# Kernel optimization log

Measured on AMD Instinct MI355X. Metric: run time of the kernel, lower is better.

## Reference

```python
import jax, jax.numpy as jnp
import numpy as np

A_, BS, T, V, E, H, NA = 8, 32, 256, 128, 512, 512, 64

def setup_inputs() -> dict:
    key = jax.random.key(0)
    ks = jax.random.split(key, 6)
    def w(k, shape, fan):
        return (jax.random.normal(k, shape, jnp.float32) / np.sqrt(fan)).astype(jnp.float32)
    return {
        "x": jax.random.normal(ks[0], (A_, BS, T, V), jnp.float32),
        "hidden_states": jnp.zeros((A_, BS, 1, H), jnp.float32),
        "enc_w": w(ks[1], (E, V), V),
        "enc_b": jnp.zeros((E,), jnp.float32),
        "w_ih": w(ks[2], (3 * H, E), E),
        "w_hh": w(ks[3], (3 * H, H), H),
        "b_ih": jnp.zeros((3 * H,), jnp.float32),
        "b_hh": jnp.zeros((3 * H,), jnp.float32),
        "dec_w": w(ks[4], (NA, H), H),
        "dec_b": jnp.zeros((NA,), jnp.float32),
    }

def _gru_scan(enc_t, h0, w_ih, w_hh, b_ih, b_hh):
    # enc_t: [T, N, E], h0: [N, H]. PyTorch GRUCell gate order: r, z, n.
    gi_all = jnp.einsum('tne,ge->tng', enc_t, w_ih) + b_ih  # precompute input projections
    def step(h, gi):
        gh = h @ w_hh.T + b_hh
        i_r, i_z, i_n = jnp.split(gi, 3, axis=-1)
        h_r, h_z, h_n = jnp.split(gh, 3, axis=-1)
        r = jax.nn.sigmoid(i_r + h_r)
        z = jax.nn.sigmoid(i_z + h_z)
        n = jnp.tanh(i_n + r * h_n)
        h_new = (1.0 - z) * n + z * h
        return h_new, h_new
    _, hs = jax.lax.scan(step, h0, gi_all)
    return hs  # [T, N, H]

def reference(x, hidden_states, enc_w, enc_b, w_ih, w_hh, b_ih, b_hh, dec_w, dec_b):
    a, bs, t, v = x.shape
    Hh = hidden_states.shape[-1]
    # MLP encoder: Linear + ReLU over feature dim
    enc = jax.nn.relu(jnp.einsum('abtv,ev->abte', x, enc_w) + enc_b)  # [a,bs,t,E]
    enc_t = enc.reshape(a * bs, t, -1).transpose(1, 0, 2)             # [t, N, E]
    h0 = hidden_states.reshape(a * bs, Hh)
    hs = _gru_scan(enc_t, h0, w_ih, w_hh, b_ih, b_hh)                 # [t, N, H]
    h = hs.transpose(1, 0, 2).reshape(a, bs, t, Hh)                   # [a,bs,t,H]
    f = jax.nn.relu(jnp.einsum('abth,nh->abtn', h, dec_w) + dec_b)    # decoder
    pi = jax.nn.softmax(f, axis=-1)                                   # softmax over v-dim
    return pi, h
```

## Files before the change

### kernel.cpp

```cpp
#include <hip/hip_runtime.h>
#include <hip/hip_bf16.h>

typedef __bf16 bf16x8 __attribute__((ext_vector_type(8)));
typedef float f32x4 __attribute__((ext_vector_type(4)));
typedef unsigned short ushort8 __attribute__((ext_vector_type(8)));
typedef float float4v __attribute__((ext_vector_type(4)));
typedef unsigned long long u64;
typedef unsigned int u32;

#define DEVI __device__ __forceinline__

#define NSEQ 256
#define TT 256
#define VV 128
#define EE 512
#define HH 512
#define NA 64
#define MROWS 65536
#define G3 1536

DEVI unsigned short f2bf(float f) {
  union { float f; unsigned u; } v; v.f = f;
  unsigned r = v.u + 0x7fffu + ((v.u >> 16) & 1u);
  return (unsigned short)(r >> 16);
}
DEVI float bf2f(unsigned short s) {
  union { unsigned u; float f; } v; v.u = ((unsigned)s) << 16;
  return v.f;
}
DEVI bf16x8 ld_bf8_g(const unsigned short* p) {
  ushort8 v = *(const ushort8*)p;
  return __builtin_bit_cast(bf16x8, v);
}
DEVI bf16x8 ld_bf8_b(const char* base, unsigned byte) {
  ushort8 v = *(const ushort8*)(base + byte);
  return __builtin_bit_cast(bf16x8, v);
}
DEVI void gload_lds16(const void* g, unsigned short* lds_base, unsigned lds_byte_off) {
  __builtin_amdgcn_global_load_lds(
      (const __attribute__((address_space(1))) unsigned int*)g,
      (__attribute__((address_space(3))) unsigned int*)(void*)((char*)lds_base + lds_byte_off),
      16, 0, 0);
}

__global__ void cast_f32_bf16(const float* __restrict__ src, unsigned short* __restrict__ dst, int n) {
  int i = blockIdx.x * blockDim.x + threadIdx.x;
  int stride = gridDim.x * blockDim.x;
  for (; i < n; i += stride) dst[i] = f2bf(src[i]);
}

__global__ void zero_u32(u32* __restrict__ p, int n) {
  int i = blockIdx.x * blockDim.x + threadIdx.x;
  if (i < n) p[i] = 0u;
}

template<bool RELU>
__global__ __launch_bounds__(256)
void gemm_bt(const unsigned short* __restrict__ A, const unsigned short* __restrict__ W,
             const float* __restrict__ bias, unsigned short* __restrict__ C,
             int N, int K) {
  __shared__ unsigned short sA[128 * 64];
  __shared__ unsigned short sB[128 * 64];
  const int tid = threadIdx.x;
  const int w = tid >> 6, lane = tid & 63;
  const int l15 = lane & 15, l4 = lane >> 4;
  const int nbn = N >> 7;
  const int bm = blockIdx.x / nbn, bn = blockIdx.x % nbn;

  f32x4 acc[4][4];
  const f32x4 fz = {0.f, 0.f, 0.f, 0.f};
#pragma unroll
  for (int i = 0; i < 4; i++)
#pragma unroll
    for (int j = 0; j < 4; j++) acc[i][j] = fz;

  const int nk = K >> 6;
  for (int bk = 0; bk < nk; ++bk) {
#pragma unroll
    for (int it = 0; it < 4; ++it) {
      int slot = it * 256 + tid;
      int row = slot >> 3, c16 = slot & 7;
      const unsigned short* ga = A + (size_t)(bm * 128 + row) * K + bk * 64 + c16 * 8;
      const unsigned short* gb = W + (size_t)(bn * 128 + row) * K + bk * 64 + c16 * 8;
      unsigned ldsoff = (unsigned)(it * 256 + w * 64) * 16;
      gload_lds16(ga, sA, ldsoff);
      gload_lds16(gb, sB, ldsoff);
    }
    __syncthreads();
#pragma unroll
    for (int kt = 0; kt < 2; ++kt) {
      bf16x8 af[4], bfr[4];
#pragma unroll
      for (int m = 0; m < 4; m++) {
        int row = ((w >> 1) * 64) + m * 16 + l15;
        af[m] = ld_bf8_g(&sA[row * 64 + kt * 32 + l4 * 8]);
      }
#pragma unroll
      for (int n = 0; n < 4; n++) {
        int row = ((w & 1) * 64) + n * 16 + l15;
        bfr[n] = ld_bf8_g(&sB[row * 64 + kt * 32 + l4 * 8]);
      }
#pragma unroll
      for (int m = 0; m < 4; m++)
#pragma unroll
        for (int n = 0; n < 4; n++)
          acc[m][n] = __builtin_amdgcn_mfma_f32_16x16x32_bf16(af[m], bfr[n], acc[m][n], 0, 0, 0);
    }
    __syncthreads();
  }

  const int r0 = bm * 128 + (w >> 1) * 64;
  const int c0 = bn * 128 + (w & 1) * 64;
#pragma unroll
  for (int n = 0; n < 4; n++) {
    int c = c0 + n * 16 + l15;
    float b = bias[c];
#pragma unroll
    for (int m = 0; m < 4; m++)
#pragma unroll
      for (int j = 0; j < 4; j++) {
        int r = r0 + m * 16 + l4 * 4 + j;
        float v = acc[m][n][j] + b;
        if (RELU) v = fmaxf(v, 0.f);
        C[(size_t)r * N + c] = f2bf(v);
      }
  }
}

#define GRU_LDS_BYTES (96 * 1024 + 64)

__global__ __launch_bounds__(256, 1)
void gru_scan(const unsigned short* __restrict__ whh,
              const float* __restrict__ b_hh,
              const unsigned short* __restrict__ gi,
              const float* __restrict__ h0f,
              unsigned short* __restrict__ hbA,
              unsigned short* __restrict__ hbB,
              float* __restrict__ hout,
              u32* __restrict__ flags) {
  extern __shared__ char lds[];
  unsigned short* sW = (unsigned short*)lds;
  u32* sCtl = (u32*)(lds + 96 * 1024);

  const int tid = threadIdx.x;
  const int w = tid >> 6, lane = tid & 63, l15 = lane & 15, l4 = lane >> 4;
  const int sg = blockIdx.x >> 4, cg = blockIdx.x & 15;
  const int s0 = sg * 32;
  const int c0 = cg * 32;
  const int mm = w >> 1, e = w & 1;

  for (int it = 0; it < 24; ++it) {
    int slot = it * 256 + tid;
    int lcr = slot >> 6, c16 = slot & 63;
    int grow = (lcr >> 5) * 512 + c0 + (lcr & 31);
    ushort8 v = *(const ushort8*)(whh + (size_t)grow * 512 + c16 * 8);
    unsigned byte = ((unsigned)(lcr * 1024 + c16 * 16)) ^ ((unsigned)(lcr & 7) << 4);
    *(ushort8*)((char*)sW + byte) = v;
  }
  if (tid <= 8) sCtl[tid] = 0;

  const int c = c0 + e * 16 + l15;
  int rj[4];
#pragma unroll
  for (int j = 0; j < 4; ++j) rj[j] = s0 + mm * 16 + l4 * 4 + j;
  float bias0 = b_hh[c], bias1 = b_hh[512 + c], bias2 = b_hh[1024 + c];
  float hp[4];
#pragma unroll
  for (int j = 0; j < 4; ++j) hp[j] = h0f[(size_t)rj[j] * HH + c];
  size_t houtb[4], gib[4];
#pragma unroll
  for (int j = 0; j < 4; ++j) {
    houtb[j] = (size_t)rj[j] * TT * HH + c;
    gib[j]   = (size_t)rj[j] * TT * G3 + c;
  }
  const int arow = s0 + mm * 16 + l15;
  const unsigned storej = (l15 & 1);

  u32* myflag = flags + sg * 32 + cg;
  const u32* pollp = flags + sg * 32 + l15;

  u32 gnext[12];
#pragma unroll
  for (int j = 0; j < 4; ++j) {
    const unsigned short* gp = gi + gib[j];
    gnext[j * 3 + 0] = gp[0];
    gnext[j * 3 + 1] = gp[512];
    gnext[j * 3 + 2] = gp[1024];
  }

  __syncthreads();

#pragma unroll 1
  for (int t = 0; t < TT; ++t) {
    const unsigned short* rb = (t & 1) ? hbA : hbB;
    unsigned short* wb = (t & 1) ? hbB : hbA;

    if (t > 0) {
      if (w == 0) {
        for (;;) {
          u32 v = __hip_atomic_load(pollp, __ATOMIC_RELAXED, __HIP_MEMORY_SCOPE_AGENT);
          int mv = (int)v;
#pragma unroll
          for (int msk = 1; msk <= 8; msk <<= 1) {
            int o = __shfl_xor(mv, msk);
            mv = mv < o ? mv : o;
          }
          if (mv >= t) break;
          __builtin_amdgcn_s_sleep(2);
        }
        __hip_atomic_store(&sCtl[8], (u32)t, __ATOMIC_RELAXED, __HIP_MEMORY_SCOPE_WORKGROUP);
      } else {
        while (__hip_atomic_load(&sCtl[8], __ATOMIC_RELAXED, __HIP_MEMORY_SCOPE_WORKGROUP) < (u32)t) {}
      }
      __builtin_amdgcn_sched_barrier(0);
    }

    const unsigned short* ap = rb + (size_t)arow * HH + l4 * 8;
    u64 av[32];
#pragma unroll
    for (int ktg = 0; ktg < 16; ++ktg) {
      av[2 * ktg]     = __hip_atomic_load((const u64*)(ap + ktg * 32),
                                          __ATOMIC_RELAXED, __HIP_MEMORY_SCOPE_AGENT);
      av[2 * ktg + 1] = __hip_atomic_load((const u64*)(ap + ktg * 32 + 4),
                                          __ATOMIC_RELAXED, __HIP_MEMORY_SCOPE_AGENT);
    }

    float gv0[4], gv1[4], gv2[4];
#pragma unroll
    for (int j = 0; j < 4; ++j) {
      gv0[j] = bf2f((unsigned short)gnext[j * 3 + 0]);
      gv1[j] = bf2f((unsigned short)gnext[j * 3 + 1]);
      gv2[j] = bf2f((unsigned short)gnext[j * 3 + 2]);
    }

    {
      int tn = (t + 1 < TT) ? t + 1 : t;
#pragma unroll
      for (int j = 0; j < 4; ++j) {
        const unsigned short* gp = gi + gib[j] + (size_t)tn * G3;
        gnext[j * 3 + 0] = gp[0];
        gnext[j * 3 + 1] = gp[512];
        gnext[j * 3 + 2] = gp[1024];
      }
    }

    f32x4 acc[3];
    const f32x4 fz = {0.f, 0.f, 0.f, 0.f};
    acc[0] = fz; acc[1] = fz; acc[2] = fz;
#pragma unroll
    for (int ktg = 0; ktg < 16; ++ktg) {
      union { u64 q[2]; bf16x8 v; } ua;
      ua.q[0] = av[2 * ktg]; ua.q[1] = av[2 * ktg + 1];
      bf16x8 a = ua.v;
#pragma unroll
      for (int g = 0; g < 3; ++g) {
        int lcr = g * 32 + e * 16 + l15;
        unsigned byte = ((unsigned)(lcr * 1024 + ktg * 64 + l4 * 16)) ^ ((unsigned)(lcr & 7) << 4);
        bf16x8 b = ld_bf8_b((const char*)sW, byte);
        acc[g] = __builtin_amdgcn_mfma_f32_16x16x32_bf16(a, b, acc[g], 0, 0, 0);
      }
    }

    float hn[4];
#pragma unroll
    for (int j = 0; j < 4; ++j) {
      float gh0 = acc[0][j] + bias0;
      float gh1 = acc[1][j] + bias1;
      float gh2 = acc[2][j] + bias2;
      float rr = 1.f / (1.f + __expf(-(gv0[j] + gh0)));
      float zz = 1.f / (1.f + __expf(-(gv1[j] + gh1)));
      float nx = gv2[j] + rr * gh2;
      float ex = __expf(2.f * nx);
      float nn = 1.f - 2.f / (ex + 1.f);
      hn[j] = (1.f - zz) * nn + zz * hp[j];
      hp[j] = hn[j];
    }

#pragma unroll
    for (int j = 0; j < 4; ++j) {
      u32 my = f2bf(hn[j]);
      u32 oth = (u32)__shfl_xor((int)my, 1);
      u32 word = (l15 & 1) ? ((oth & 0xffffu) | (my << 16))
                           : ((my & 0xffffu) | (oth << 16));
      if ((unsigned)(j >> 1) == storej) {
        u32* dst = (u32*)(wb + (size_t)rj[j] * HH + (c & ~1));
        __hip_atomic_store(dst, word, __ATOMIC_RELAXED, __HIP_MEMORY_SCOPE_AGENT);
      }
    }

    asm volatile("s_waitcnt vmcnt(0)" ::: "memory");
    __hip_atomic_store(&sCtl[w], (u32)(t + 1), __ATOMIC_RELAXED, __HIP_MEMORY_SCOPE_WORKGROUP);
    if (w == 0) {
      u32 mt;
      do {
        u32 tv = __hip_atomic_load(&sCtl[lane & 3], __ATOMIC_RELAXED, __HIP_MEMORY_SCOPE_WORKGROUP);
        mt = tv;
#pragma unroll
        for (int msk = 1; msk <= 2; msk <<= 1) {
          u32 o = (u32)__shfl_xor((int)mt, msk);
          mt = mt < o ? mt : o;
        }
      } while (mt < (u32)(t + 1));
      if (lane == 0)
        __hip_atomic_store(myflag, (u32)(t + 1), __ATOMIC_RELAXED, __HIP_MEMORY_SCOPE_AGENT);
    }

#pragma unroll
    for (int j = 0; j < 4; ++j)
      hout[houtb[j] + (size_t)t * HH] = hn[j];
  }
}

__global__ __launch_bounds__(256)
void decoder_softmax(const float* __restrict__ hf,
                     const unsigned short* __restrict__ dwb,
                     const float* __restrict__ dec_b,
                     float* __restrict__ pi) {
  __shared__ unsigned short sH[64 * 512];
  const int tid = threadIdx.x, w = tid >> 6, lane = tid & 63, l15 = lane & 15, l4 = lane >> 4;
  const size_t m0 = (size_t)blockIdx.x * 64;

#pragma unroll
  for (int it = 0; it < 16; ++it) {
    int slot = it * 256 + tid;
    int row = slot >> 6, c16 = slot & 63;
    const float* g = hf + (m0 + row) * 512 + c16 * 8;
    float4v v0 = *(const float4v*)g;
    float4v v1 = *(const float4v*)(g + 4);
    ushort8 u;
    u[0] = f2bf(v0[0]); u[1] = f2bf(v0[1]); u[2] = f2bf(v0[2]); u[3] = f2bf(v0[3]);
    u[4] = f2bf(v1[0]); u[5] = f2bf(v1[1]); u[6] = f2bf(v1[2]); u[7] = f2bf(v1[3]);
    unsigned byte = ((unsigned)(row * 1024 + c16 * 16)) ^ ((unsigned)(row & 7) << 4);
    *(ushort8*)((char*)sH + byte) = u;
  }
  __syncthreads();

  f32x4 acc[4];
  const f32x4 fz = {0.f, 0.f, 0.f, 0.f};
#pragma unroll
  for (int n = 0; n < 4; n++) acc[n] = fz;

  for (int kt = 0; kt < 16; ++kt) {
    int row = w * 16 + l15;
    unsigned byte = ((unsigned)(row * 1024 + kt * 64 + l4 * 16)) ^ ((unsigned)(row & 7) << 4);
    bf16x8 a = ld_bf8_b((const char*)sH, byte);
#pragma unroll
    for (int nt = 0; nt < 4; nt++) {
      bf16x8 b = ld_bf8_g(dwb + (size_t)(nt * 16 + l15) * 512 + kt * 32 + l4 * 8);
      acc[nt] = __builtin_amdgcn_mfma_f32_16x16x32_bf16(a, b, acc[nt], 0, 0, 0);
    }
  }

#pragma unroll
  for (int j = 0; j < 4; j++) {
    size_t r = m0 + w * 16 + l4 * 4 + j;
    float v[4];
    float mx = -1e30f;
#pragma unroll
    for (int nt = 0; nt < 4; nt++) {
      v[nt] = fmaxf(acc[nt][j] + dec_b[nt * 16 + l15], 0.f);
      mx = fmaxf(mx, v[nt]);
    }
#pragma unroll
    for (int msk = 1; msk <= 8; msk <<= 1) mx = fmaxf(mx, __shfl_xor(mx, msk));
    float s = 0.f;
#pragma unroll
    for (int nt = 0; nt < 4; nt++) { v[nt] = __expf(v[nt] - mx); s += v[nt]; }
#pragma unroll
    for (int msk = 1; msk <= 8; msk <<= 1) s += __shfl_xor(s, msk);
    float inv = 1.f / s;
#pragma unroll
    for (int nt = 0; nt < 4; nt++) pi[r * 64 + nt * 16 + l15] = v[nt] * inv;
  }
}

extern "C" void kernel_launch(void* const* d_in, const int* in_sizes, int n_in,
                              void* d_out, int out_size, void* d_ws, size_t ws_size,
                              hipStream_t stream) {
  const float* x     = (const float*)d_in[0];
  const float* h0    = (const float*)d_in[1];
  const float* enc_w = (const float*)d_in[2];
  const float* enc_b = (const float*)d_in[3];
  const float* w_ih  = (const float*)d_in[4];
  const float* w_hh  = (const float*)d_in[5];
  const float* b_ih  = (const float*)d_in[6];
  const float* b_hh  = (const float*)d_in[7];
  const float* dec_w = (const float*)d_in[8];
  const float* dec_b = (const float*)d_in[9];

  float* pi_out = (float*)d_out;
  float* h_out  = (float*)d_out + 4194304;

  unsigned short* ws = (unsigned short*)d_ws;
  size_t off = 0;
  unsigned short* x_bf    = ws + off; off += (size_t)MROWS * VV;
  unsigned short* enc_bf  = ws + off; off += (size_t)MROWS * EE;
  unsigned short* gi_bf   = ws + off; off += (size_t)MROWS * G3;
  unsigned short* encw_bf = ws + off; off += (size_t)EE * VV;
  unsigned short* wih_bf  = ws + off; off += (size_t)G3 * EE;
  unsigned short* whh_bf  = ws + off; off += (size_t)G3 * HH;
  unsigned short* decw_bf = ws + off; off += (size_t)NA * HH;
  unsigned short* hb0     = ws + off; off += (size_t)NSEQ * HH;
  unsigned short* hb1     = ws + off; off += (size_t)NSEQ * HH;
  u32* flags = (u32*)((((uintptr_t)(ws + off)) + 255) & ~(uintptr_t)255);
  (void)ws_size; (void)in_sizes; (void)n_in; (void)out_size;

  hipFuncSetAttribute((const void*)gru_scan,
                      hipFuncAttributeMaxDynamicSharedMemorySize, GRU_LDS_BYTES);

  auto cast = [&](const float* s, unsigned short* d, int n) {
    int blocks = (n + 255) / 256; if (blocks > 2048) blocks = 2048;
    cast_f32_bf16<<<blocks, 256, 0, stream>>>(s, d, n);
  };
  cast(x, x_bf, MROWS * VV);
  cast(enc_w, encw_bf, EE * VV);
  cast(w_ih, wih_bf, G3 * EE);
  cast(w_hh, whh_bf, G3 * HH);
  cast(dec_w, decw_bf, NA * HH);
  cast(h0, hb1, NSEQ * HH);

  zero_u32<<<1, 256, 0, stream>>>(flags, 256);

  gemm_bt<true><<<(MROWS / 128) * (EE / 128), 256, 0, stream>>>(x_bf, encw_bf, enc_b, enc_bf, EE, VV);
  gemm_bt<false><<<(MROWS / 128) * (G3 / 128), 256, 0, stream>>>(enc_bf, wih_bf, b_ih, gi_bf, G3, EE);

  gru_scan<<<dim3(128), dim3(256), GRU_LDS_BYTES, stream>>>(
      whh_bf, b_hh, gi_bf, h0, hb0, hb1, h_out, flags);

  decoder_softmax<<<1024, 256, 0, stream>>>(h_out, decw_bf, dec_b, pi_out);
}
```

Measured before the change: 1.829 ms.

## Use per-chunk readiness polling and LDS-buffered hidden-state output in GRU scan

Result: faster. 1.707 ms (-6.7%).

```diff
diff --git a/kernel.cpp b/kernel.cpp
--- a/kernel.cpp
+++ b/kernel.cpp
@@ -5,6 +5,7 @@
 typedef float f32x4 __attribute__((ext_vector_type(4)));
 typedef unsigned short ushort8 __attribute__((ext_vector_type(8)));
 typedef float float4v __attribute__((ext_vector_type(4)));
+typedef unsigned int uint4v __attribute__((ext_vector_type(4)));
 typedef unsigned long long u64;
 typedef unsigned int u32;
 
@@ -41,6 +42,10 @@
       (const __attribute__((address_space(1))) unsigned int*)g,
       (__attribute__((address_space(3))) unsigned int*)(void*)((char*)lds_base + lds_byte_off),
       16, 0, 0);
+}
+DEVI void ld_chunk_sc(uint4v* dst, const void* p) {
+  asm volatile("global_load_dwordx4 %0, %1, off sc0 sc1"
+               : "=&v"(*dst) : "v"((u64)p) : "memory");
 }
 
 __global__ void cast_f32_bf16(const float* __restrict__ src, unsigned short* __restrict__ dst, int n) {
@@ -127,7 +132,7 @@
   }
 }
 
-#define GRU_LDS_BYTES (96 * 1024 + 64)
+#define GRU_LDS_BYTES (96 * 1024 + 32 * 1024 + 64)
 
 __global__ __launch_bounds__(256, 1)
 void gru_scan(const unsigned short* __restrict__ whh,
@@ -140,7 +145,8 @@
               u32* __restrict__ flags) {
   extern __shared__ char lds[];
   unsigned short* sW = (unsigned short*)lds;
-  u32* sCtl = (u32*)(lds + 96 * 1024);
+  float* sRing = (float*)(lds + 96 * 1024);
+  u32* sCtl = (u32*)(lds + 128 * 1024);
 
   const int tid = threadIdx.x;
   const int w = tid >> 6, lane = tid & 63, l15 = lane & 15, l4 = lane >> 4;
@@ -157,7 +163,7 @@
     unsigned byte = ((unsigned)(lcr * 1024 + c16 * 16)) ^ ((unsigned)(lcr & 7) << 4);
     *(ushort8*)((char*)sW + byte) = v;
   }
-  if (tid <= 8) sCtl[tid] = 0;
+  if (tid < 4) sCtl[tid] = 0;
 
   const int c = c0 + e * 16 + l15;
   int rj[4];
@@ -179,7 +185,7 @@
   u32* myflag = flags + sg * 32 + cg;
   const u32* pollp = flags + sg * 32 + l15;
 
-  u32 gnext[12];
+  unsigned short gnext[12];
 #pragma unroll
   for (int j = 0; j < 4; ++j) {
     const unsigned short* gp = gi + gib[j];
@@ -195,43 +201,35 @@
     const unsigned short* rb = (t & 1) ? hbA : hbB;
     unsigned short* wb = (t & 1) ? hbB : hbA;
 
-    if (t > 0) {
-      if (w == 0) {
-        for (;;) {
-          u32 v = __hip_atomic_load(pollp, __ATOMIC_RELAXED, __HIP_MEMORY_SCOPE_AGENT);
-          int mv = (int)v;
-#pragma unroll
-          for (int msk = 1; msk <= 8; msk <<= 1) {
-            int o = __shfl_xor(mv, msk);
-            mv = mv < o ? mv : o;
-          }
-          if (mv >= t) break;
-          __builtin_amdgcn_s_sleep(2);
-        }
-        __hip_atomic_store(&sCtl[8], (u32)t, __ATOMIC_RELAXED, __HIP_MEMORY_SCOPE_WORKGROUP);
-      } else {
-        while (__hip_atomic_load(&sCtl[8], __ATOMIC_RELAXED, __HIP_MEMORY_SCOPE_WORKGROUP) < (u32)t) {}
-      }
-      __builtin_amdgcn_sched_barrier(0);
-    }
-
-    const unsigned short* ap = rb + (size_t)arow * HH + l4 * 8;
-    u64 av[32];
-#pragma unroll
-    for (int ktg = 0; ktg < 16; ++ktg) {
-      av[2 * ktg]     = __hip_atomic_load((const u64*)(ap + ktg * 32),
-                                          __ATOMIC_RELAXED, __HIP_MEMORY_SCOPE_AGENT);
-      av[2 * ktg + 1] = __hip_atomic_load((const u64*)(ap + ktg * 32 + 4),
-                                          __ATOMIC_RELAXED, __HIP_MEMORY_SCOPE_AGENT);
-    }
-
     float gv0[4], gv1[4], gv2[4];
 #pragma unroll
     for (int j = 0; j < 4; ++j) {
-      gv0[j] = bf2f((unsigned short)gnext[j * 3 + 0]);
-      gv1[j] = bf2f((unsigned short)gnext[j * 3 + 1]);
-      gv2[j] = bf2f((unsigned short)gnext[j * 3 + 2]);
-    }
+      gv0[j] = bf2f(gnext[j * 3 + 0]);
+      gv1[j] = bf2f(gnext[j * 3 + 1]);
+      gv2[j] = bf2f(gnext[j * 3 + 2]);
+    }
+
+    const char* abase = (const char*)(rb + (size_t)arow * HH) + l4 * 16;
+    uint4v av4[16];
+    u32 mask;
+    {
+      u32 fv = __hip_atomic_load(pollp, __ATOMIC_RELAXED, __HIP_MEMORY_SCOPE_AGENT);
+      u64 bal = __ballot(fv >= (u32)t);
+      mask = (u32)(bal & 0xffffu);
+    }
+#pragma unroll
+    for (int i = 0; i < 16; ++i) {
+      int ktg = (cg + i) & 15;
+      while (!((mask >> ktg) & 1u)) {
+        __builtin_amdgcn_s_sleep(1);
+        u32 fv = __hip_atomic_load(pollp, __ATOMIC_RELAXED, __HIP_MEMORY_SCOPE_AGENT);
+        u64 bal = __ballot(fv >= (u32)t);
+        mask = (u32)(bal & 0xffffu);
+      }
+      ld_chunk_sc(&av4[i], abase + (size_t)ktg * 64);
+    }
+    asm volatile("s_waitcnt vmcnt(0)" ::: "memory");
+    __builtin_amdgcn_sched_barrier(0);
 
     {
       int tn = (t + 1 < TT) ? t + 1 : t;
@@ -248,10 +246,9 @@
     const f32x4 fz = {0.f, 0.f, 0.f, 0.f};
     acc[0] = fz; acc[1] = fz; acc[2] = fz;
 #pragma unroll
-    for (int ktg = 0; ktg < 16; ++ktg) {
-      union { u64 q[2]; bf16x8 v; } ua;
-      ua.q[0] = av[2 * ktg]; ua.q[1] = av[2 * ktg + 1];
-      bf16x8 a = ua.v;
+    for (int i = 0; i < 16; ++i) {
+      int ktg = (cg + i) & 15;
+      bf16x8 a = __builtin_bit_cast(bf16x8, av4[i]);
 #pragma unroll
       for (int g = 0; g < 3; ++g) {
         int lcr = g * 32 + e * 16 + l15;
@@ -305,9 +302,21 @@
         __hip_atomic_store(myflag, (u32)(t + 1), __ATOMIC_RELAXED, __HIP_MEMORY_SCOPE_AGENT);
     }
 
-#pragma unroll
-    for (int j = 0; j < 4; ++j)
-      hout[houtb[j] + (size_t)t * HH] = hn[j];
+    {
+      float* slot = sRing + (((t & 7) * 256 + tid) << 2);
+#pragma unroll
+      for (int j = 0; j < 4; ++j) slot[j] = hn[j];
+    }
+    if ((t & 7) == 7) {
+      int tb = t - 7;
+#pragma unroll
+      for (int tt = 0; tt < 8; ++tt) {
+        const float* src = sRing + ((tt * 256 + tid) << 2);
+#pragma unroll
+        for (int j = 0; j < 4; ++j)
+          hout[houtb[j] + (size_t)(tb + tt) * HH] = src[j];
+      }
+    }
   }
 }
 
```
